# Optimization experiments

Measured on AMD Instinct MI355X. Metric: run time of the kernel, lower is better.

## Reference

```python
import jax, jax.numpy as jnp
import numpy as np


def setup_inputs() -> dict:
    key = jax.random.key(0)
    k1, k2 = jax.random.split(key)
    B, C, H, W, D = 4, 32, 256, 512, 48
    h1 = jax.random.normal(k1, (B, C, H, W), dtype=jnp.float32)
    cost = jax.random.normal(k2, (B, D, H, W), dtype=jnp.float32)
    return {"h1": h1, "cost": cost}


def reference(h1, cost):
    # g2[b,c,h,w] = sum_d cost[b,d,h,w] * stop_grad(h1)[b,c,h,w+d]  for w+d < W
    # (original torch code detaches h1, so grads only flow through cost)
    B, C, H, W = h1.shape
    D = cost.shape[1]
    h1d = jax.lax.stop_gradient(h1)
    w_idx = jnp.arange(W)

    # scan over disparity levels; each step does a masked roll + fused MAC,
    # never materializing the [B,C,D,H,W] shifted stack.
    cost_d_major = jnp.moveaxis(cost, 1, 0)  # [D,B,H,W]

    def step(acc, xd):
        d, c_d = xd  # c_d: [B,H,W]
        valid = (w_idx < (W - d)).astype(h1.dtype)  # [W]; zero beyond W-d
        shifted = jnp.roll(h1d, -d, axis=-1) * valid  # h1[..., w+d], zero-padded
        acc = acc + c_d[:, None, :, :] * shifted  # broadcast over C
        return acc, None

    g2, _ = jax.lax.scan(step, jnp.zeros_like(h1), (jnp.arange(D), cost_d_major))
    return g2
```

## Files before the change

### kernel.cpp

```cpp
#include <hip/hip_runtime.h>


#define BB 4
#define CC 32
#define HH 256
#define WW 512
#define DDISP 48
#define HW (HH * WW)
#define TW 256
#define NT 256

__device__ __forceinline__ void ldh(const float* __restrict__ row, int wq,
                                    float* __restrict__ dst)
{
    int wc = wq > (WW - 4) ? (WW - 4) : wq;
    float4 t = *(const float4*)(row + wc);
    bool ok = wq < WW;
    dst[0] = ok ? t.x : 0.f;
    dst[1] = ok ? t.y : 0.f;
    dst[2] = ok ? t.z : 0.f;
    dst[3] = ok ? t.w : 0.f;
}

__global__ __launch_bounds__(NT, 4)
void dense_warp_kernel(const float* __restrict__ h1,
                       const float* __restrict__ cost,
                       float* __restrict__ out)
{
    const int blk    = blockIdx.x;
    const int wside  = blk & 1;
    const int h      = (blk >> 1) & (HH - 1);
    const int cgrp   = (blk >> 9) & 3;
    const int b      = blk >> 11;
    const int wstart = wside * TW;

    const int lane = threadIdx.x & 63;
    const int wid  = threadIdx.x >> 6;
    const int c0   = (cgrp << 3) + (wid << 1);
    const int w0   = lane << 2;
    const int wq0  = wstart + w0;

    const float* r0 = h1 + (((size_t)b * CC + c0    ) * HH + h) * WW;
    const float* r1 = h1 + (((size_t)b * CC + c0 + 1) * HH + h) * WW;

    float acc0[4] = {0.f, 0.f, 0.f, 0.f};
    float acc1[4] = {0.f, 0.f, 0.f, 0.f};

    float win0[8], win1[8];
    ldh(r0, wq0,     &win0[0]);  ldh(r0, wq0 + 4, &win0[4]);
    ldh(r1, wq0,     &win1[0]);  ldh(r1, wq0 + 4, &win1[4]);

    const float* cp = cost + ((size_t)b * DDISP * HH + h) * WW + wq0;

#pragma unroll
    for (int g = 0; g < 12; ++g) {
        const int P = g & 1;
        float cv[4][4];
#pragma unroll
        for (int dd = 0; dd < 4; ++dd) {
            float4 t = *(const float4*)(cp + (size_t)(4 * g + dd) * HW);
            cv[dd][0] = t.x; cv[dd][1] = t.y; cv[dd][2] = t.z; cv[dd][3] = t.w;
        }
#pragma unroll
        for (int dd = 0; dd < 4; ++dd)
#pragma unroll
            for (int j = 0; j < 4; ++j) {
                const int o    = dd + j;
                const int slot = (P + (o >> 2)) & 1;
                acc0[j] += cv[dd][j] * win0[slot * 4 + (o & 3)];
                acc1[j] += cv[dd][j] * win1[slot * 4 + (o & 3)];
            }
        ldh(r0, wq0 + 4 * g + 8, &win0[P * 4]);
        ldh(r1, wq0 + 4 * g + 8, &win1[P * 4]);
    }

    float* o0 = out + (((size_t)b * CC + c0    ) * HH + h) * WW + wq0;
    float* o1 = out + (((size_t)b * CC + c0 + 1) * HH + h) * WW + wq0;
    *(float4*)o0 = make_float4(acc0[0], acc0[1], acc0[2], acc0[3]);
    *(float4*)o1 = make_float4(acc1[0], acc1[1], acc1[2], acc1[3]);
}

extern "C" void kernel_launch(void* const* d_in, const int* in_sizes, int n_in,
                              void* d_out, int out_size, void* d_ws, size_t ws_size,
                              hipStream_t stream) {
    const float* h1   = (const float*)d_in[0];
    const float* cost = (const float*)d_in[1];
    float* out        = (float*)d_out;
    dim3 grid(BB * HH * 2 * 4);
    dense_warp_kernel<<<grid, NT, 0, stream>>>(h1, cost, out);
}
```

Before: 282.4 us.

## Process four channels per wave, prefetch cost, specialize unmasked half, nontemporal stores

Each wave now computes four channels instead of two, so every cost load is reused across twice as many channels and the cost traffic per output drops. The grid is halved to match, and blocks are reordered so neighbouring blocks share (b,h) rows for L2 locality. Cost vectors are double-buffered to prefetch the next disparity group, and the left half uses a template without the bounds mask. Outputs are written with nontemporal stores. Register pressure rises with 16 accumulators and 32 window values, which may hurt occupancy under launch_bounds(256,4).

Result: slower. 469.6 us (+66.2%).

```diff
diff --git a/kernel.cpp b/kernel.cpp
--- a/kernel.cpp
+++ b/kernel.cpp
@@ -10,16 +10,103 @@
 #define TW 256
 #define NT 256
 
-__device__ __forceinline__ void ldh(const float* __restrict__ row, int wq,
+typedef float f32x4 __attribute__((ext_vector_type(4)));
+
+template<bool MASK>
+__device__ __forceinline__ void ldq(const float* __restrict__ row, int wq,
                                     float* __restrict__ dst)
 {
-    int wc = wq > (WW - 4) ? (WW - 4) : wq;
-    float4 t = *(const float4*)(row + wc);
-    bool ok = wq < WW;
-    dst[0] = ok ? t.x : 0.f;
-    dst[1] = ok ? t.y : 0.f;
-    dst[2] = ok ? t.z : 0.f;
-    dst[3] = ok ? t.w : 0.f;
+    if (MASK) {
+        int wc = wq > (WW - 4) ? (WW - 4) : wq;
+        float4 t = *(const float4*)(row + wc);
+        bool ok = wq < WW;
+        dst[0] = ok ? t.x : 0.f;
+        dst[1] = ok ? t.y : 0.f;
+        dst[2] = ok ? t.z : 0.f;
+        dst[3] = ok ? t.w : 0.f;
+    } else {
+        float4 t = *(const float4*)(row + wq);
+        dst[0] = t.x; dst[1] = t.y; dst[2] = t.z; dst[3] = t.w;
+    }
+}
+
+template<bool MASK>
+__device__ __forceinline__ void body(const float* __restrict__ h1,
+                                     const float* __restrict__ cost,
+                                     float* __restrict__ out,
+                                     int b, int h, int cgrp, int wstart)
+{
+    const int lane = threadIdx.x & 63;
+    const int wid  = threadIdx.x >> 6;
+    const int c0   = (cgrp << 4) + (wid << 2);
+    const int w0   = lane << 2;
+    const int wq0  = wstart + w0;
+
+    const float* r[4];
+#pragma unroll
+    for (int c = 0; c < 4; ++c)
+        r[c] = h1 + (((size_t)(b * CC + c0 + c)) * HH + h) * WW;
+
+    float acc[4][4];
+#pragma unroll
+    for (int c = 0; c < 4; ++c)
+#pragma unroll
+        for (int j = 0; j < 4; ++j) acc[c][j] = 0.f;
+
+    float win[4][8];
+#pragma unroll
+    for (int c = 0; c < 4; ++c) {
+        ldq<false>(r[c], wq0, &win[c][0]);
+        ldq<MASK >(r[c], wq0 + 4, &win[c][4]);
+    }
+
+    const float* cp = cost + ((size_t)(b * DDISP) * HH + h) * WW + wq0;
+
+    float cv[2][4][4];
+#pragma unroll
+    for (int dd = 0; dd < 4; ++dd) {
+        float4 t = *(const float4*)(cp + (size_t)dd * HW);
+        cv[0][dd][0] = t.x; cv[0][dd][1] = t.y;
+        cv[0][dd][2] = t.z; cv[0][dd][3] = t.w;
+    }
+
+#pragma unroll
+    for (int g = 0; g < 12; ++g) {
+        const int cur = g & 1;
+        const int nxt = cur ^ 1;
+        if (g < 11) {
+#pragma unroll
+            for (int dd = 0; dd < 4; ++dd) {
+                float4 t = *(const float4*)(cp + (size_t)(4 * (g + 1) + dd) * HW);
+                cv[nxt][dd][0] = t.x; cv[nxt][dd][1] = t.y;
+                cv[nxt][dd][2] = t.z; cv[nxt][dd][3] = t.w;
+            }
+        }
+#pragma unroll
+        for (int c = 0; c < 4; ++c)
+#pragma unroll
+            for (int dd = 0; dd < 4; ++dd)
+#pragma unroll
+                for (int j = 0; j < 4; ++j) {
+                    const int o    = dd + j;
+                    const int slot = (cur + (o >> 2)) & 1;
+                    acc[c][j] = __builtin_fmaf(cv[cur][dd][j],
+                                               win[c][slot * 4 + (o & 3)],
+                                               acc[c][j]);
+                }
+        if (g < 11) {
+#pragma unroll
+            for (int c = 0; c < 4; ++c)
+                ldq<MASK>(r[c], wq0 + 4 * g + 8, &win[c][cur * 4]);
+        }
+    }
+
+    float* ob = out + (((size_t)(b * CC + c0)) * HH + h) * WW + wq0;
+#pragma unroll
+    for (int c = 0; c < 4; ++c) {
+        f32x4 v = { acc[c][0], acc[c][1], acc[c][2], acc[c][3] };
+        __builtin_nontemporal_store(v, (f32x4*)(ob + (size_t)c * HW));
+    }
 }
 
 __global__ __launch_bounds__(NT, 4)
@@ -27,57 +114,16 @@
                        const float* __restrict__ cost,
                        float* __restrict__ out)
 {
-    const int blk    = blockIdx.x;
-    const int wside  = blk & 1;
-    const int h      = (blk >> 1) & (HH - 1);
-    const int cgrp   = (blk >> 9) & 3;
-    const int b      = blk >> 11;
-    const int wstart = wside * TW;
+    const int blk  = blockIdx.x;
+    const int blk2 = blk & 2047;
+    const int sub  = blk2 & 7;
+    const int cgrp = (blk2 >> 3) & 1;
+    const int tile = ((blk2 >> 4) << 3) | sub;
+    const int b    = tile >> 8;
+    const int h    = tile & 255;
 
-    const int lane = threadIdx.x & 63;
-    const int wid  = threadIdx.x >> 6;
-    const int c0   = (cgrp << 3) + (wid << 1);
-    const int w0   = lane << 2;
-    const int wq0  = wstart + w0;
-
-    const float* r0 = h1 + (((size_t)b * CC + c0    ) * HH + h) * WW;
-    const float* r1 = h1 + (((size_t)b * CC + c0 + 1) * HH + h) * WW;
-
-    float acc0[4] = {0.f, 0.f, 0.f, 0.f};
-    float acc1[4] = {0.f, 0.f, 0.f, 0.f};
-
-    float win0[8], win1[8];
-    ldh(r0, wq0,     &win0[0]);  ldh(r0, wq0 + 4, &win0[4]);
-    ldh(r1, wq0,     &win1[0]);  ldh(r1, wq0 + 4, &win1[4]);
-
-    const float* cp = cost + ((size_t)b * DDISP * HH + h) * WW + wq0;
-
-#pragma unroll
-    for (int g = 0; g < 12; ++g) {
-        const int P = g & 1;
-        float cv[4][4];
-#pragma unroll
-        for (int dd = 0; dd < 4; ++dd) {
-            float4 t = *(const float4*)(cp + (size_t)(4 * g + dd) * HW);
-            cv[dd][0] = t.x; cv[dd][1] = t.y; cv[dd][2] = t.z; cv[dd][3] = t.w;
-        }
-#pragma unroll
-        for (int dd = 0; dd < 4; ++dd)
-#pragma unroll
-            for (int j = 0; j < 4; ++j) {
-                const int o    = dd + j;
-                const int slot = (P + (o >> 2)) & 1;
-                acc0[j] += cv[dd][j] * win0[slot * 4 + (o & 3)];
-                acc1[j] += cv[dd][j] * win1[slot * 4 + (o & 3)];
-            }
-        ldh(r0, wq0 + 4 * g + 8, &win0[P * 4]);
-        ldh(r1, wq0 + 4 * g + 8, &win1[P * 4]);
-    }
-
-    float* o0 = out + (((size_t)b * CC + c0    ) * HH + h) * WW + wq0;
-    float* o1 = out + (((size_t)b * CC + c0 + 1) * HH + h) * WW + wq0;
-    *(float4*)o0 = make_float4(acc0[0], acc0[1], acc0[2], acc0[3]);
-    *(float4*)o1 = make_float4(acc1[0], acc1[1], acc1[2], acc1[3]);
+    if (blk < 2048) body<false>(h1, cost, out, b, h, cgrp, 0);
+    else            body<true >(h1, cost, out, b, h, cgrp, TW);
 }
 
 extern "C" void kernel_launch(void* const* d_in, const int* in_sizes, int n_in,
@@ -86,6 +132,6 @@
     const float* h1   = (const float*)d_in[0];
     const float* cost = (const float*)d_in[1];
     float* out        = (float*)d_out;
-    dim3 grid(BB * HH * 2 * 4);
+    dim3 grid(BB * HH * 2 * 2);
     dense_warp_kernel<<<grid, NT, 0, stream>>>(h1, cost, out);
 }
```
